# Performance work log

Hardware: AMD Instinct MI355X
Metric: run time of the kernel (lower is better)

Reference implementation:

```python
import jax, jax.numpy as jnp
import numpy as np

C = 51  # num_relation


def setup_inputs() -> dict:
    key = jax.random.key(0)
    N_o, N_u, D = 16384, 16384, 1024
    k = jax.random.split(key, 6)
    feat = jax.random.normal(k[0], (N_o + N_u, D), jnp.float32)
    # first N_o rows are labeled (label != 0), remaining N_u rows unlabeled (label == 0)
    label = jnp.concatenate([
        jax.random.randint(k[1], (N_o,), 1, C),
        jnp.zeros((N_u,), jnp.int32),
    ]).astype(jnp.int32)
    W_o = jax.random.normal(k[2], (C, D), jnp.float32) * 0.03
    b_o = jnp.zeros((C,), jnp.float32)
    W = jax.random.normal(k[3], (C, D), jnp.float32) * 0.03
    b = jnp.zeros((C,), jnp.float32)
    cls = jnp.arange(C)
    group_mid_mask = (cls >= 16) & (cls < 36)   # groups[1]
    group_tail_mask = cls >= 36                 # groups[2]
    # runtime torch.randint partner sampling, hoisted to input construction
    idx_m = jax.random.randint(k[4], (2, N_u), 0, N_o)  # 2 mid copies
    idx_t = jax.random.randint(k[5], (3, N_u), 0, N_o)  # 3 tail copies
    return dict(feat=feat, label=label, W_o=W_o, b_o=b_o, W=W, b=b,
                group_mid_mask=group_mid_mask, group_tail_mask=group_tail_mask,
                idx_m=idx_m, idx_t=idx_t)


def reference(feat, label, W_o, b_o, W, b, group_mid_mask, group_tail_mask, idx_m, idx_t):
    n_u = idx_m.shape[1]
    n_o = feat.shape[0] - n_u
    feat_o, feat_u = feat[:n_o], feat[n_o:]
    label_o = label[:n_o]

    # fc_o under no_grad, then softmax / top-1 rank + score
    logits = jax.lax.stop_gradient(feat_u @ W_o.T + b_o)      # [N_u, C]
    p = jax.nn.softmax(logits, axis=1)
    pred = jnp.argmax(p, axis=1)                               # ranks[:,0]
    score = jnp.max(p, axis=1)                                 # score[:,0]

    # group membership + confidence thresholds (heads are unused in the original)
    mid_m = group_mid_mask[pred] & (score > 0.5)
    tail_m = group_tail_mask[pred] & (score > 0.3)

    oh_u = jax.nn.one_hot(pred, C, dtype=feat.dtype)
    oh_o = jax.nn.one_hot(label_o, C, dtype=feat.dtype)

    im = idx_m.reshape(-1)   # [2*N_u]
    it = idx_t.reshape(-1)   # [3*N_u]

    fm = 0.7 * feat_o[im] + 0.3 * jnp.tile(feat_u, (2, 1))
    lm = 0.7 * oh_o[im] + 0.3 * jnp.tile(oh_u, (2, 1))
    ft = 0.7 * feat_o[it] + 0.3 * jnp.tile(feat_u, (3, 1))
    lt = 0.7 * oh_o[it] + 0.3 * jnp.tile(oh_u, (3, 1))

    feat_cat = jnp.concatenate([fm, ft], axis=0)               # [5*N_u, D]
    label_cat = jnp.concatenate([lm, lt], axis=0)              # [5*N_u, C]
    w = jnp.concatenate([jnp.tile(mid_m, 2), jnp.tile(tail_m, 3)]).astype(feat.dtype)

    # soft-label cross entropy on fc(feat_cat); masked mean over selected rows
    logp = jax.nn.log_softmax(feat_cat @ W.T + b, axis=1)
    ce = -(logp * label_cat).sum(axis=1)
    cnt = w.sum()
    return (ce * w).sum() / jnp.maximum(cnt, 1.0)
```

## Files before the change

kernel.cpp:

```cpp
#include <hip/hip_runtime.h>
#include <math.h>

#define DD 1024
#define NU 16384
#define NO 16384
#define NCEB 320

typedef short short8 __attribute__((ext_vector_type(8)));
typedef float f32x4 __attribute__((ext_vector_type(4)));

__device__ __forceinline__ unsigned short f2b(float x) {
    unsigned int u = __float_as_uint(x);
    u += 0x7FFFu + ((u >> 16) & 1u);
    return (unsigned short)(u >> 16);
}

__device__ __forceinline__ short8 cvt8(float4 a, float4 b) {
    short8 r;
    r[0] = (short)f2b(a.x); r[1] = (short)f2b(a.y);
    r[2] = (short)f2b(a.z); r[3] = (short)f2b(a.w);
    r[4] = (short)f2b(b.x); r[5] = (short)f2b(b.y);
    r[6] = (short)f2b(b.z); r[7] = (short)f2b(b.w);
    return r;
}

__device__ __forceinline__ void gl_lds(const void* g, void* l) {
    __builtin_amdgcn_global_load_lds(
        (const __attribute__((address_space(1))) void*)g,
        (__attribute__((address_space(3))) void*)l, 16, 0, 0);
}

__global__ __launch_bounds__(256) void convW(const float* __restrict__ W_o,
                                             unsigned short* __restrict__ Wcat,
                                             double* __restrict__ gnum,
                                             int* __restrict__ gcnt,
                                             int* __restrict__ gdone) {
    if (blockIdx.x == 0 && threadIdx.x == 0) {
        gnum[0] = 0.0; gcnt[0] = 0; gdone[0] = 0;
    }
    const int n = blockIdx.x;
    const int k = threadIdx.x * 4;
    const float* src = (n < 51) ? (W_o + (size_t)n * DD) : nullptr;
    float4 v = src ? *(const float4*)(src + k) : make_float4(0.f, 0.f, 0.f, 0.f);
    ushort4 o;
    o.x = f2b(v.x); o.y = f2b(v.y); o.z = f2b(v.z); o.w = f2b(v.w);
    *(ushort4*)(Wcat + (size_t)n * DD + k) = o;
}

__global__ __launch_bounds__(256, 4) void gemm_u(const float* __restrict__ feat,
                                                 const unsigned short* __restrict__ Wcat,
                                                 const float* __restrict__ b_o,
                                                 int* __restrict__ flags) {
    __shared__ __attribute__((aligned(16))) char lds[3 * 12288];
    const int m0 = blockIdx.x * 64;
    const int tid = threadIdx.x;
    const int lane = tid & 63;
    const int w = tid >> 6;
    const int m = lane & 15;
    const int quad = lane >> 4;
    const int s = m & 7;
    const int s2 = m & 3;

    const char *gs0, *gs1, *gs2;
    int lo0, lo1, lo2;
    { const int r = w * 16 + (lane >> 3);
      const int g = (lane & 7) ^ (r & 7);
      gs0 = (const char*)(feat + (size_t)(NO + m0 + r) * DD + g * 4); lo0 = (w * 2) * 1024; }
    { const int r = w * 16 + 8 + (lane >> 3);
      const int g = (lane & 7) ^ (r & 7);
      gs1 = (const char*)(feat + (size_t)(NO + m0 + r) * DD + g * 4); lo1 = (w * 2 + 1) * 1024; }
    { const int r = w * 16 + (lane >> 2);
      const int g = (lane & 3) ^ (r & 3);
      gs2 = (const char*)(Wcat + (size_t)r * DD + g * 8); lo2 = 8192 + w * 1024; }

    f32x4 acc[4];
#pragma unroll
    for (int nf = 0; nf < 4; ++nf) acc[nf] = (f32x4){0.f, 0.f, 0.f, 0.f};

    const int rA = w * 16 + m;

#define STAGE(t, buf)                                  \
    do {                                               \
        gl_lds(gs0 + (size_t)(t) * 128, (buf) + lo0);  \
        gl_lds(gs1 + (size_t)(t) * 128, (buf) + lo1);  \
        gl_lds(gs2 + (size_t)(t) * 64,  (buf) + lo2);  \
    } while (0)

    STAGE(0, lds);
    STAGE(1, lds + 12288);

    int bc = 0;
    for (int kt = 0; kt < 32; ++kt) {
        if (kt < 30) {
            const int bi2 = (bc == 0) ? 2 : bc - 1;
            STAGE(kt + 2, lds + bi2 * 12288);
            asm volatile("s_waitcnt vmcnt(6)\n\ts_barrier" ::: "memory");
        } else if (kt == 30) {
            asm volatile("s_waitcnt vmcnt(3)\n\ts_barrier" ::: "memory");
        } else {
            asm volatile("s_waitcnt vmcnt(0)\n\ts_barrier" ::: "memory");
        }
        const char* buf = lds + bc * 12288;
        const float4 f0 = *(const float4*)(buf + rA * 128 + ((2 * quad) ^ s) * 16);
        const float4 f1 = *(const float4*)(buf + rA * 128 + ((2 * quad + 1) ^ s) * 16);
        const short8 af = cvt8(f0, f1);
#pragma unroll
        for (int nf = 0; nf < 4; ++nf) {
            const short8 bf =
                *(const short8*)(buf + 8192 + (m + nf * 16) * 64 + (quad ^ s2) * 16);
            acc[nf] = __builtin_amdgcn_mfma_f32_16x16x32_bf16(af, bf, acc[nf], 0, 0, 0);
        }
        bc = (bc == 2) ? 0 : bc + 1;
    }
#undef STAGE

    const int rloc = m0 + w * 16 + quad * 4;
    float boc[4];
#pragma unroll
    for (int c = 0; c < 4; ++c) {
        const int col = c * 16 + m;
        boc[c] = (col < 51) ? b_o[col] : 0.f;
    }
#pragma unroll
    for (int r = 0; r < 4; ++r) {
        float z[4];
        float mx = acc[0][r] + boc[0];
        int mi = m;
        z[0] = mx;
#pragma unroll
        for (int c = 1; c < 4; ++c) {
            const int col = c * 16 + m;
            z[c] = (col < 51) ? acc[c][r] + boc[c] : -INFINITY;
            if (z[c] > mx) { mx = z[c]; mi = col; }
        }
#pragma unroll
        for (int off = 1; off < 16; off <<= 1) {
            const float om = __shfl_xor(mx, off);
            const int oi = __shfl_xor(mi, off);
            if (om > mx || (om == mx && oi < mi)) { mx = om; mi = oi; }
        }
        float e = 0.f;
#pragma unroll
        for (int c = 0; c < 4; ++c)
            if (c * 16 + m < 51) e += expf(z[c] - mx);
#pragma unroll
        for (int off = 1; off < 16; off <<= 1) e += __shfl_xor(e, off);
        const float score = 1.f / e;
        const int mid = (mi >= 16 && mi < 36 && score > 0.5f) ? 1 : 0;
        const int tail = (mi >= 36 && score > 0.3f) ? 1 : 0;
        if (m == 0) flags[rloc + r] = mi | (mid << 8) | (tail << 9);
    }
}

__global__ __launch_bounds__(256) void cekernel(const float* __restrict__ feat,
                                                const float* __restrict__ W,
                                                const float* __restrict__ bb,
                                                const int* __restrict__ label,
                                                const int* __restrict__ idxm,
                                                const int* __restrict__ idxt,
                                                const int* __restrict__ flags,
                                                double* __restrict__ gnum,
                                                int* __restrict__ gcnt,
                                                int* __restrict__ gdone,
                                                float* __restrict__ out) {
    __shared__ float snum[4];
    __shared__ int scnt[4];
    const int w = threadIdx.x >> 6;
    const int lane = threadIdx.x & 63;
    const int j = (blockIdx.x * 4 + w) * 64 + lane;
    int u, o, fl, act;
    if (j < 2 * NU) {
        u = j & (NU - 1);
        fl = flags[u];
        act = (fl >> 8) & 1;
        o = idxm[j];
    } else {
        const int j2 = j - 2 * NU;
        u = j2 & (NU - 1);
        fl = flags[u];
        act = (fl >> 9) & 1;
        o = idxt[j2];
    }
    const float bbv = (lane < 51) ? bb[lane] : 0.f;
    unsigned long long mask = __ballot(act);
    float fsum = 0.f;
    int ccnt = 0;
    while (mask) {
        const int bpos = (int)__builtin_ctzll(mask);
        mask &= mask - 1;
        const int ob = __shfl(o, bpos);
        const int ub = __shfl(u, bpos);
        const int pu = __shfl(fl, bpos) & 255;
        const f32x4* fo4 = (const f32x4*)(feat + (size_t)ob * DD);
        const f32x4* fu4 = (const f32x4*)(feat + (size_t)(NO + ub) * DD);
        f32x4 g[4];
#pragma unroll
        for (int t = 0; t < 4; ++t)
            g[t] = 0.7f * fo4[t * 64 + lane] + 0.3f * fu4[t * 64 + lane];
        float zmy = 0.f;
        for (int c = 0; c < 51; ++c) {
            const f32x4* wr = (const f32x4*)(W + (size_t)c * DD);
            f32x4 p = wr[lane] * g[0];
            p += wr[64 + lane] * g[1];
            p += wr[128 + lane] * g[2];
            p += wr[192 + lane] * g[3];
            float d = (p[0] + p[1]) + (p[2] + p[3]);
#pragma unroll
            for (int off = 1; off < 64; off <<= 1) d += __shfl_xor(d, off);
            if (lane == c) zmy = d;
        }
        const float z = (lane < 51) ? zmy + bbv : -INFINITY;
        float mx = z;
#pragma unroll
        for (int off = 1; off < 64; off <<= 1) mx = fmaxf(mx, __shfl_xor(mx, off));
        float e = (lane < 51) ? expf(z - mx) : 0.f;
#pragma unroll
        for (int off = 1; off < 64; off <<= 1) e += __shfl_xor(e, off);
        const float lse = mx + logf(e);
        const int lo = label[ob];
        const float zlo = __shfl(z, lo);
        const float zpu = __shfl(z, pu);
        fsum += lse - 0.7f * zlo - 0.3f * zpu;
        ++ccnt;
    }
    if (lane == 0) { snum[w] = fsum; scnt[w] = ccnt; }
    __syncthreads();
    if (threadIdx.x == 0) {
        const float bn = snum[0] + snum[1] + snum[2] + snum[3];
        const int bcnt = scnt[0] + scnt[1] + scnt[2] + scnt[3];
        if (bcnt > 0) {
            atomicAdd(gnum, (double)bn);
            atomicAdd(gcnt, bcnt);
        }
        __threadfence();
        const int dn = atomicAdd(gdone, 1);
        if (dn == NCEB - 1) {
            const double n = atomicAdd(gnum, 0.0);
            const int cc = atomicAdd(gcnt, 0);
            out[0] = (float)(n / (cc > 1 ? (double)cc : 1.0));
        }
    }
}

extern "C" void kernel_launch(void* const* d_in, const int* in_sizes, int n_in,
                              void* d_out, int out_size, void* d_ws, size_t ws_size,
                              hipStream_t stream) {
    const float* feat = (const float*)d_in[0];
    const int* label = (const int*)d_in[1];
    const float* W_o = (const float*)d_in[2];
    const float* b_o = (const float*)d_in[3];
    const float* W = (const float*)d_in[4];
    const float* b = (const float*)d_in[5];
    const int* idxm = (const int*)d_in[8];
    const int* idxt = (const int*)d_in[9];

    char* ws = (char*)d_ws;
    int* flags = (int*)ws;
    unsigned short* Wcat = (unsigned short*)(ws + 65536);
    double* gnum = (double*)(ws + 196608);
    int* gcnt = (int*)(ws + 196616);
    int* gdone = (int*)(ws + 196620);

    convW<<<64, 256, 0, stream>>>(W_o, Wcat, gnum, gcnt, gdone);
    gemm_u<<<256, 256, 0, stream>>>(feat, Wcat, b_o, flags);
    cekernel<<<NCEB, 256, 0, stream>>>(feat, W, b, label, idxm, idxt, flags,
                                       gnum, gcnt, gdone, (float*)d_out);
}
```

Baseline: 239.1 us.

## Compact active mixup rows into a work list for load-balanced CE kernel

The classifier kernel now appends each active (partner, unlabeled row, pseudo-label) pair to a global list through an atomic counter, instead of writing per-row flags. The CE kernel walks this compacted list with a grid-stride loop over waves, and the grid shrinks to 256 blocks. This is meant to remove the imbalance where some waves held many active rows in their ballot mask while others held none. It adds one global atomic per active entry and makes the order of the floating-point accumulation nondeterministic.

```diff
diff --git a/kernel.cpp b/kernel.cpp
--- a/kernel.cpp
+++ b/kernel.cpp
@@ -4,7 +4,7 @@
 #define DD 1024
 #define NU 16384
 #define NO 16384
-#define NCEB 320
+#define NCEB 256
 
 typedef short short8 __attribute__((ext_vector_type(8)));
 typedef float f32x4 __attribute__((ext_vector_type(4)));
@@ -32,11 +32,12 @@
 
 __global__ __launch_bounds__(256) void convW(const float* __restrict__ W_o,
                                              unsigned short* __restrict__ Wcat,
+                                             int* __restrict__ cnt,
                                              double* __restrict__ gnum,
                                              int* __restrict__ gcnt,
                                              int* __restrict__ gdone) {
     if (blockIdx.x == 0 && threadIdx.x == 0) {
-        gnum[0] = 0.0; gcnt[0] = 0; gdone[0] = 0;
+        cnt[0] = 0; gnum[0] = 0.0; gcnt[0] = 0; gdone[0] = 0;
     }
     const int n = blockIdx.x;
     const int k = threadIdx.x * 4;
@@ -50,7 +51,10 @@
 __global__ __launch_bounds__(256, 4) void gemm_u(const float* __restrict__ feat,
                                                  const unsigned short* __restrict__ Wcat,
                                                  const float* __restrict__ b_o,
-                                                 int* __restrict__ flags) {
+                                                 const int* __restrict__ idxm,
+                                                 const int* __restrict__ idxt,
+                                                 int* __restrict__ cnt,
+                                                 int2* __restrict__ list) {
     __shared__ __attribute__((aligned(16))) char lds[3 * 12288];
     const int m0 = blockIdx.x * 64;
     const int tid = threadIdx.x;
@@ -148,7 +152,14 @@
         const float score = 1.f / e;
         const int mid = (mi >= 16 && mi < 36 && score > 0.5f) ? 1 : 0;
         const int tail = (mi >= 36 && score > 0.3f) ? 1 : 0;
-        if (m == 0) flags[rloc + r] = mi | (mid << 8) | (tail << 9);
+        const int nref = mid ? 2 : (tail ? 3 : 0);
+        if (m < nref) {
+            const int u = rloc + r;
+            const int oo = mid ? idxm[(size_t)m * NU + u]
+                               : idxt[(size_t)m * NU + u];
+            const int p = atomicAdd(cnt, 1);
+            list[p] = make_int2(oo, u | (mi << 16));
+        }
     }
 }
 
@@ -156,9 +167,8 @@
                                                 const float* __restrict__ W,
                                                 const float* __restrict__ bb,
                                                 const int* __restrict__ label,
-                                                const int* __restrict__ idxm,
-                                                const int* __restrict__ idxt,
-                                                const int* __restrict__ flags,
+                                                const int* __restrict__ cnt,
+                                                const int2* __restrict__ list,
                                                 double* __restrict__ gnum,
                                                 int* __restrict__ gcnt,
                                                 int* __restrict__ gdone,
@@ -167,36 +177,21 @@
     __shared__ int scnt[4];
     const int w = threadIdx.x >> 6;
     const int lane = threadIdx.x & 63;
-    const int j = (blockIdx.x * 4 + w) * 64 + lane;
-    int u, o, fl, act;
-    if (j < 2 * NU) {
-        u = j & (NU - 1);
-        fl = flags[u];
-        act = (fl >> 8) & 1;
-        o = idxm[j];
-    } else {
-        const int j2 = j - 2 * NU;
-        u = j2 & (NU - 1);
-        fl = flags[u];
-        act = (fl >> 9) & 1;
-        o = idxt[j2];
-    }
+    const int n = cnt[0];
     const float bbv = (lane < 51) ? bb[lane] : 0.f;
-    unsigned long long mask = __ballot(act);
     float fsum = 0.f;
     int ccnt = 0;
-    while (mask) {
-        const int bpos = (int)__builtin_ctzll(mask);
-        mask &= mask - 1;
-        const int ob = __shfl(o, bpos);
-        const int ub = __shfl(u, bpos);
-        const int pu = __shfl(fl, bpos) & 255;
+    for (int t = blockIdx.x * 4 + w; t < n; t += NCEB * 4) {
+        const int2 e = list[t];
+        const int ob = e.x;
+        const int ub = e.y & 0xFFFF;
+        const int pu = e.y >> 16;
         const f32x4* fo4 = (const f32x4*)(feat + (size_t)ob * DD);
         const f32x4* fu4 = (const f32x4*)(feat + (size_t)(NO + ub) * DD);
         f32x4 g[4];
 #pragma unroll
-        for (int t = 0; t < 4; ++t)
-            g[t] = 0.7f * fo4[t * 64 + lane] + 0.3f * fu4[t * 64 + lane];
+        for (int q = 0; q < 4; ++q)
+            g[q] = 0.7f * fo4[q * 64 + lane] + 0.3f * fu4[q * 64 + lane];
         float zmy = 0.f;
         for (int c = 0; c < 51; ++c) {
             const f32x4* wr = (const f32x4*)(W + (size_t)c * DD);
@@ -213,10 +208,10 @@
         float mx = z;
 #pragma unroll
         for (int off = 1; off < 64; off <<= 1) mx = fmaxf(mx, __shfl_xor(mx, off));
-        float e = (lane < 51) ? expf(z - mx) : 0.f;
-#pragma unroll
-        for (int off = 1; off < 64; off <<= 1) e += __shfl_xor(e, off);
-        const float lse = mx + logf(e);
+        float e2 = (lane < 51) ? expf(z - mx) : 0.f;
+#pragma unroll
+        for (int off = 1; off < 64; off <<= 1) e2 += __shfl_xor(e2, off);
+        const float lse = mx + logf(e2);
         const int lo = label[ob];
         const float zlo = __shfl(z, lo);
         const float zpu = __shfl(z, pu);
@@ -235,9 +230,9 @@
         __threadfence();
         const int dn = atomicAdd(gdone, 1);
         if (dn == NCEB - 1) {
-            const double n = atomicAdd(gnum, 0.0);
+            const double nn = atomicAdd(gnum, 0.0);
             const int cc = atomicAdd(gcnt, 0);
-            out[0] = (float)(n / (cc > 1 ? (double)cc : 1.0));
+            out[0] = (float)(nn / (cc > 1 ? (double)cc : 1.0));
         }
     }
 }
@@ -255,14 +250,15 @@
     const int* idxt = (const int*)d_in[9];
 
     char* ws = (char*)d_ws;
-    int* flags = (int*)ws;
-    unsigned short* Wcat = (unsigned short*)(ws + 65536);
-    double* gnum = (double*)(ws + 196608);
-    int* gcnt = (int*)(ws + 196616);
-    int* gdone = (int*)(ws + 196620);
-
-    convW<<<64, 256, 0, stream>>>(W_o, Wcat, gnum, gcnt, gdone);
-    gemm_u<<<256, 256, 0, stream>>>(feat, Wcat, b_o, flags);
-    cekernel<<<NCEB, 256, 0, stream>>>(feat, W, b, label, idxm, idxt, flags,
+    unsigned short* Wcat = (unsigned short*)ws;
+    int* cntp = (int*)(ws + 131072);
+    double* gnum = (double*)(ws + 131088);
+    int* gcnt = (int*)(ws + 131096);
+    int* gdone = (int*)(ws + 131100);
+    int2* list = (int2*)(ws + 131104);
+
+    convW<<<64, 256, 0, stream>>>(W_o, Wcat, cntp, gnum, gcnt, gdone);
+    gemm_u<<<256, 256, 0, stream>>>(feat, Wcat, b_o, idxm, idxt, cntp, list);
+    cekernel<<<NCEB, 256, 0, stream>>>(feat, W, b, label, cntp, list,
                                        gnum, gcnt, gdone, (float*)d_out);
 }
```

Result: faster. 231.8 us (-3.1%).
